# Kernel tuning notes

Hardware: AMD Instinct MI355X
Metric: run time of the kernel (lower is better)

## Reference

```python
import jax, jax.numpy as jnp
import numpy as np
import itertools

N_OBJECTS = 6  # subsets of range(6), sizes 1..6 -> 63 subsets

def _subset_groups():
    # group subsets by length so each group runs as one batched LSTM
    groups = {}
    for m in range(1, N_OBJECTS + 1):
        for s in itertools.combinations(range(6), m):
            groups.setdefault(m, []).append(list(s))
    return [(m, np.asarray(v, dtype=np.int32)) for m, v in groups.items()]

SUBSET_GROUPS = _subset_groups()


def _lstm_final_h(x, W_ih, W_hh, b_ih, b_hh):
    """x: [B,T,D] -> final hidden state [B,H]. PyTorch gate order i,f,g,o."""
    H = W_hh.shape[1]
    B = x.shape[0]
    # precompute input projections for all timesteps: [B,T,4H]
    xz = jnp.einsum('btd,gd->btg', x, W_ih) + b_ih + b_hh

    def step(carry, xt):
        h, c = carry
        z = xt + h @ W_hh.T
        i, f, g, o = jnp.split(z, 4, axis=-1)
        c = jax.nn.sigmoid(f) * c + jax.nn.sigmoid(i) * jnp.tanh(g)
        h = jax.nn.sigmoid(o) * jnp.tanh(c)
        return (h, c), None

    h0 = jnp.zeros((B, H), x.dtype)
    (h, _), _ = jax.lax.scan(step, (h0, h0), jnp.swapaxes(xz, 0, 1))
    return h


def setup_inputs() -> dict:
    key = jax.random.key(0)
    ks = jax.random.split(key, 10)
    D, H, FC, A = 16, 128, 256, 10
    mb = 8192
    s = lambda k, shape, fan: jax.random.normal(k, shape, jnp.float32) * (1.0 / np.sqrt(fan))
    return {
        'x_input': jax.random.normal(ks[0], (mb, 6, D), jnp.float32),
        'W_ih': s(ks[1], (4 * H, D), D),
        'W_hh': s(ks[2], (4 * H, H), H),
        'b_ih': jnp.zeros((4 * H,), jnp.float32),
        'b_hh': jnp.zeros((4 * H,), jnp.float32),
        'fc1_W': s(ks[3], (FC, H), H),
        'fc1_b': jnp.zeros((FC,), jnp.float32),
        'fc2_W': s(ks[4], (A, FC), FC),
        'fc2_b': jnp.zeros((A,), jnp.float32),
    }


def reference(x_input, W_ih, W_hh, b_ih, b_hh, fc1_W, fc1_b, fc2_W, fc2_b):
    mb = x_input.shape[0]
    H = W_hh.shape[1]
    hs = []
    # subsets of the same length are batched into one LSTM pass (fused form of
    # the original 63-iteration python loop); aggregation is permutation-invariant
    for m, idx in SUBSET_GROUPS:
        nL = idx.shape[0]
        xg = x_input[:, idx, :]                       # [mb, nL, m, D] gather
        xg = xg.reshape(mb * nL, m, x_input.shape[-1])
        h = _lstm_final_h(xg, W_ih, W_hh, b_ih, b_hh)  # [mb*nL, H]
        hs.append(h.reshape(mb, nL, H))
    holder = jnp.concatenate(hs, axis=1)              # [mb, 63, H]
    x = jnp.max(holder, axis=1)                       # aggregate == 'max'
    x = jax.nn.relu(x @ fc1_W.T + fc1_b)
    x = x @ fc2_W.T + fc2_b
    return jax.nn.log_softmax(x, axis=-1)
```

## Files before the change

kernel.cpp:

```cpp
#include <hip/hip_runtime.h>
#include <hip/hip_bf16.h>

#define BLOCK   512
#define NSAMP   16
#define HDIM    128
#define DDIM    16
#define NOBJ    6
#define NSLOT   16

typedef __attribute__((ext_vector_type(8))) short bf16x8;
typedef __attribute__((ext_vector_type(4))) float f32x4;

constexpr int pc6(int m)  { int c = 0; for (int i = 0; i < 6; ++i) c += (m >> i) & 1; return c; }
constexpr int msb6(int m) { int b = -1; for (int i = 0; i < 6; ++i) if (m & (1 << i)) b = i; return b; }

struct NodeRec { int jo, ps, sl; };
struct Plan { int cnt[7]; int n1[7]; NodeRec nd[7][20]; };
constexpr Plan make_plan() {
    Plan P{};
    int slotOf[64] = {};
    bool busy[NSLOT] = {};
    for (int d = 1; d <= 6; ++d) {
        int n = 0;
        for (int M = 1; M < 64; ++M) {
            if (pc6(M) != d || msb6(M) != 5) continue;
            P.nd[d][n].jo = 5;
            P.nd[d][n].ps = (d == 1) ? -1 : slotOf[M & ~(1 << 5)];
            P.nd[d][n].sl = -1;
            ++n;
        }
        int pend[20] = {}; int np = 0;
        for (int M = 1; M < 64; ++M) {
            if (pc6(M) != d || msb6(M) >= 5) continue;
            const int hi = msb6(M);
            int fs = -1;
            for (int s = 0; s < NSLOT; ++s) if (!busy[s]) { fs = s; break; }
            if (fs >= 0) {
                busy[fs] = true; slotOf[M] = fs;
                P.nd[d][n].jo = hi;
                P.nd[d][n].ps = (d == 1) ? -1 : slotOf[M & ~(1 << hi)];
                P.nd[d][n].sl = fs;
                ++n;
            } else pend[np++] = M;
        }
        P.n1[d] = n;
        int freeds[20] = {}; int nf = 0;
        if (d >= 2)
            for (int M = 1; M < 64; ++M)
                if (pc6(M) == d - 1 && msb6(M) == 4) freeds[nf++] = slotOf[M];
        for (int i = 0; i < np; ++i) {
            const int M = pend[i]; const int hi = msb6(M);
            const int s = freeds[--nf];
            slotOf[M] = s;
            P.nd[d][n].jo = hi;
            P.nd[d][n].ps = slotOf[M & ~(1 << hi)];
            P.nd[d][n].sl = s;
            ++n;
        }
        P.cnt[d] = n;
        for (int s = 0; s < NSLOT; ++s) busy[s] = false;
        for (int M = 1; M < 64; ++M)
            if (pc6(M) == d && msb6(M) < 5) busy[slotOf[M]] = true;
    }
    return P;
}
constexpr Plan PL = make_plan();

#define LOG2E   1.44269504f
#define TWOL2E  2.88539008f
#define SLOT_SH (16 * NSAMP * 8)

__device__ __forceinline__ unsigned short f2bf(float x) {
    union { float f; unsigned int u; } a; a.f = x;
    unsigned int r = (a.u + 0x7FFFu + ((a.u >> 16) & 1u)) >> 16;
    return (unsigned short)r;
}
__device__ __forceinline__ unsigned pk2(float a, float b) {
    union { __hip_bfloat162 h; unsigned u; } z;
    z.h = __float22bfloat162_rn(float2{a, b});
    return z.u;
}
__device__ __forceinline__ float bflo(unsigned p) {
    union { unsigned u; float f; } a; a.u = p << 16; return a.f;
}
__device__ __forceinline__ float bfhi(unsigned p) {
    union { unsigned u; float f; } a; a.u = p & 0xFFFF0000u; return a.f;
}


__global__ __launch_bounds__(BLOCK)
__attribute__((amdgpu_waves_per_eu(2, 4)))
void subset_lstm_fused_kernel(
    const float* __restrict__ x_input,
    const float* __restrict__ W_ih,
    const float* __restrict__ W_hh,
    const float* __restrict__ b_ih,
    const float* __restrict__ b_hh,
    const float* __restrict__ fc1_W,
    const float* __restrict__ fc1_b,
    const float* __restrict__ fc2_W,
    const float* __restrict__ fc2_b,
    float* __restrict__ out)
{
    __shared__ __align__(16) unsigned short hs[NSLOT * SLOT_SH];
    __shared__ __align__(16) unsigned short xb[NOBJ * 2 * NSAMP * 8];
    __shared__ __align__(16) unsigned short xpad[16];
    float* s_maxh  = (float*)hs;
    float* s_fc1   = (float*)(hs + 4096);
    float* s_logit = (float*)xb;

    const int t      = threadIdx.x;
    const int w      = t >> 6;
    const int lane   = t & 63;
    const int quad   = lane >> 4;
    const int m16    = lane & 15;
    const int s_base = blockIdx.x * NSAMP;

    if (t < 16) xpad[t] = (t == 0) ? f2bf(1.0f) : (unsigned short)0;

    for (int idx = t; idx < NOBJ * 2 * NSAMP * 8; idx += BLOCK) {
        const int j = idx & 7, n = (idx >> 3) & 15, q = (idx >> 7) & 1, obj = idx >> 8;
        xb[idx] = f2bf(x_input[(s_base + n) * (NOBJ * DDIM) + obj * DDIM + q * 8 + j]);
    }

    bf16x8 wf[4][5];
    #pragma unroll
    for (int g = 0; g < 4; ++g) {
        const float sc = (g == 2) ? TWOL2E : -LOG2E;
        const int grow = g * HDIM + w * 16 + m16;
        const float* whr = W_hh + grow * HDIM;
        const float* wir = W_ih + grow * DDIM;
        #pragma unroll
        for (int q = 0; q < 4; ++q) {
            union { unsigned short u[8]; bf16x8 v; } pk;
            #pragma unroll
            for (int j = 0; j < 8; ++j)
                pk.u[j] = f2bf(sc * whr[q * 32 + quad * 8 + j]);
            wf[g][q] = pk.v;
        }
        {
            union { unsigned short u[8]; bf16x8 v; } pk;
            #pragma unroll
            for (int j = 0; j < 8; ++j) {
                float v = 0.0f;
                if (quad < 2) v = sc * wir[quad * 8 + j];
                else if (quad == 2 && j == 0) v = sc * (b_ih[grow] + b_hh[grow]);
                pk.u[j] = f2bf(v);
            }
            wf[g][4] = pk.v;
        }
    }

    uint2 cs[NSLOT];
    float mh[4] = {-1e30f, -1e30f, -1e30f, -1e30f};
    const int kslot = w * 2 + (quad >> 1);

    #pragma unroll
    for (int d = 1; d <= 6; ++d) {
        __syncthreads();
        #pragma unroll
        for (int seg = 0; seg < 2; ++seg) {
            const int sBeg = seg ? PL.n1[d] : 0;
            const int sEnd = seg ? PL.cnt[d] : PL.n1[d];
            if (seg && sBeg >= sEnd) continue;
            if (seg) __syncthreads();

            #pragma unroll
            for (int ni = sBeg; ni < sEnd; ni += 2) {
                f32x4 acc[2][4];
                #pragma unroll
                for (int e = 0; e < 2; ++e) {
                    if (ni + e >= sEnd) continue;
                    const int jo = PL.nd[d][ni + e].jo;
                    const int ps = PL.nd[d][ni + e].ps;
                    #pragma unroll
                    for (int g = 0; g < 4; ++g)
                        acc[e][g] = f32x4{0.f, 0.f, 0.f, 0.f};
                    const unsigned short* bp = (quad < 2)
                        ? &xb[((jo * 2 + quad) * NSAMP + m16) * 8]
                        : &xpad[(quad - 2) * 8];
                    const bf16x8 bfx = *(const bf16x8*)bp;
                    #pragma unroll
                    for (int g = 0; g < 4; ++g)
                        acc[e][g] = __builtin_amdgcn_mfma_f32_16x16x32_bf16(
                            wf[g][4], bfx, acc[e][g], 0, 0, 0);
                    if (ps >= 0) {
                        #pragma unroll
                        for (int q = 0; q < 4; ++q) {
                            const bf16x8 bh = *(const bf16x8*)
                                &hs[((ps * 16 + q * 4 + quad) * NSAMP + m16) * 8];
                            #pragma unroll
                            for (int g = 0; g < 4; ++g)
                                acc[e][g] = __builtin_amdgcn_mfma_f32_16x16x32_bf16(
                                    wf[g][q], bh, acc[e][g], 0, 0, 0);
                        }
                    }
                }
                #pragma unroll
                for (int e = 0; e < 2; ++e) {
                    if (ni + e >= sEnd) continue;
                    const int ps = PL.nd[d][ni + e].ps;
                    const int sl = PL.nd[d][ni + e].sl;
                    float cn4[4], hn4[4];
                    #pragma unroll
                    for (int r = 0; r < 4; ++r) {
                        float cprev = 0.0f;
                        if (ps >= 0) {
                            const unsigned p = (r < 2) ? cs[ps].x : cs[ps].y;
                            cprev = (r & 1) ? bfhi(p) : bflo(p);
                        }
                        const float u  = 1.0f + __builtin_amdgcn_exp2f(acc[e][0][r]);
                        const float q  = 1.0f + __builtin_amdgcn_exp2f(acc[e][1][r]);
                        const float v  = 1.0f + __builtin_amdgcn_exp2f(acc[e][2][r]);
                        const float qo = 1.0f + __builtin_amdgcn_exp2f(acc[e][3][r]);
                        const float uv  = u * v;
                        const float num = fmaf(q, v - 2.0f, cprev * uv);
                        const float cn  = num * __builtin_amdgcn_rcpf(q * uv);
                        const float wt  = 1.0f + __builtin_amdgcn_exp2f(TWOL2E * cn);
                        const float h   = (wt - 2.0f) * __builtin_amdgcn_rcpf(qo * wt);
                        cn4[r] = cn; hn4[r] = h;
                        mh[r] = fmaxf(mh[r], h);
                    }
                    if (sl >= 0) {
                        cs[sl].x = pk2(cn4[0], cn4[1]);
                        cs[sl].y = pk2(cn4[2], cn4[3]);
                        union { __hip_bfloat162 h2[2]; uint2 v; } hp;
                        hp.h2[0] = __float22bfloat162_rn(float2{hn4[0], hn4[1]});
                        hp.h2[1] = __float22bfloat162_rn(float2{hn4[2], hn4[3]});
                        *(uint2*)&hs[((sl * 16 + kslot) * NSAMP + m16) * 8
                                     + (quad & 1) * 4] = hp.v;
                    }
                }
            }
        }
    }

    __syncthreads();
    {
        float4 v; v.x = mh[0]; v.y = mh[1]; v.z = mh[2]; v.w = mh[3];
        *(float4*)&s_maxh[m16 * HDIM + w * 16 + quad * 4] = v;
    }
    __syncthreads();

    {
        const int f  = t & 255;
        const int sh = t >> 8;
        float a1[8];
        #pragma unroll
        for (int s = 0; s < 8; ++s) a1[s] = fc1_b[f];
        for (int k4 = 0; k4 < HDIM / 4; ++k4) {
            const float4 wv = *(const float4*)&fc1_W[f * HDIM + k4 * 4];
            #pragma unroll
            for (int s = 0; s < 8; ++s) {
                const float4 h4 = *(const float4*)&s_maxh[(sh * 8 + s) * HDIM + k4 * 4];
                a1[s] += wv.x * h4.x + wv.y * h4.y + wv.z * h4.z + wv.w * h4.w;
            }
        }
        #pragma unroll
        for (int s = 0; s < 8; ++s)
            s_fc1[(sh * 8 + s) * 256 + f] = fmaxf(a1[s], 0.0f);
    }
    __syncthreads();

    if (t < NSAMP * 10) {
        const int s = t / 10, a = t % 10;
        float acc2 = fc2_b[a];
        for (int f4 = 0; f4 < 256 / 4; ++f4) {
            const float4 wv = *(const float4*)&fc2_W[a * 256 + f4 * 4];
            const float4 v  = *(const float4*)&s_fc1[s * 256 + f4 * 4];
            acc2 += wv.x * v.x + wv.y * v.y + wv.z * v.z + wv.w * v.w;
        }
        s_logit[s * 10 + a] = acc2;
    }
    __syncthreads();

    if (t < NSAMP) {
        float m = -1e30f;
        #pragma unroll
        for (int a = 0; a < 10; ++a) m = fmaxf(m, s_logit[t * 10 + a]);
        float sum = 0.0f;
        #pragma unroll
        for (int a = 0; a < 10; ++a) sum += __expf(s_logit[t * 10 + a] - m);
        const float lse = m + __logf(sum);
        #pragma unroll
        for (int a = 0; a < 10; ++a)
            out[(s_base + t) * 10 + a] = s_logit[t * 10 + a] - lse;
    }
}

extern "C" void kernel_launch(void* const* d_in, const int* in_sizes, int n_in,
                              void* d_out, int out_size, void* d_ws, size_t ws_size,
                              hipStream_t stream)
{
    (void)d_ws; (void)ws_size; (void)n_in; (void)out_size;

    const float* x   = (const float*)d_in[0];
    const float* Wih = (const float*)d_in[1];
    const float* Whh = (const float*)d_in[2];
    const float* bih = (const float*)d_in[3];
    const float* bhh = (const float*)d_in[4];
    const float* f1w = (const float*)d_in[5];
    const float* f1b = (const float*)d_in[6];
    const float* f2w = (const float*)d_in[7];
    const float* f2b = (const float*)d_in[8];

    const int mb = in_sizes[0] / (NOBJ * DDIM);
    dim3 grid(mb / NSAMP), block(BLOCK);
    subset_lstm_fused_kernel<<<grid, block, 0, stream>>>(
        x, Wih, Whh, bih, bhh, f1w, f1b, f2w, f2b, (float*)d_out);
}
```

Measured before the change: 204.2 us.

## Roll subset-LSTM schedule into table-driven loop with cell state in LDS

Replaces the fully unrolled compile-time plan with a rolled loop that reads packed node records from a kernel-argument table. Cell state moves from a 16-entry register array into shared memory, and the constant bias-pad row is folded into the x buffer. Nodes are now processed one at a time instead of in pairs, and the waves_per_eu hint is dropped. The aim is to cut code size and register pressure, at the cost of less MFMA interleaving between nodes plus extra LDS traffic and loop overhead.

```diff
diff --git a/kernel.cpp b/kernel.cpp
--- a/kernel.cpp
+++ b/kernel.cpp
@@ -66,9 +66,11 @@
 }
 constexpr Plan PL = make_plan();
 
+struct KTab { unsigned rec[63]; int cnt[8]; int n1[8]; };
+
 #define LOG2E   1.44269504f
 #define TWOL2E  2.88539008f
-#define SLOT_SH (16 * NSAMP * 8)
+#define SLOT_SH 2048
 
 __device__ __forceinline__ unsigned short f2bf(float x) {
     union { float f; unsigned int u; } a; a.f = x;
@@ -89,8 +91,7 @@
 
 
 __global__ __launch_bounds__(BLOCK)
-__attribute__((amdgpu_waves_per_eu(2, 4)))
-void subset_lstm_fused_kernel(
+void subset_lstm_rolled_kernel(
     const float* __restrict__ x_input,
     const float* __restrict__ W_ih,
     const float* __restrict__ W_hh,
@@ -100,11 +101,12 @@
     const float* __restrict__ fc1_b,
     const float* __restrict__ fc2_W,
     const float* __restrict__ fc2_b,
-    float* __restrict__ out)
+    float* __restrict__ out,
+    KTab tab)
 {
-    __shared__ __align__(16) unsigned short hs[NSLOT * SLOT_SH];
-    __shared__ __align__(16) unsigned short xb[NOBJ * 2 * NSAMP * 8];
-    __shared__ __align__(16) unsigned short xpad[16];
+    __shared__ __align__(16) unsigned short hs [NSLOT * SLOT_SH];
+    __shared__ __align__(16) unsigned short csb[NSLOT * SLOT_SH];
+    __shared__ __align__(16) unsigned short xb[NOBJ * 4 * NSAMP * 8];
     float* s_maxh  = (float*)hs;
     float* s_fc1   = (float*)(hs + 4096);
     float* s_logit = (float*)xb;
@@ -116,11 +118,12 @@
     const int m16    = lane & 15;
     const int s_base = blockIdx.x * NSAMP;
 
-    if (t < 16) xpad[t] = (t == 0) ? f2bf(1.0f) : (unsigned short)0;
-
-    for (int idx = t; idx < NOBJ * 2 * NSAMP * 8; idx += BLOCK) {
-        const int j = idx & 7, n = (idx >> 3) & 15, q = (idx >> 7) & 1, obj = idx >> 8;
-        xb[idx] = f2bf(x_input[(s_base + n) * (NOBJ * DDIM) + obj * DDIM + q * 8 + j]);
+    for (int idx = t; idx < NOBJ * 4 * NSAMP * 8; idx += BLOCK) {
+        const int j = idx & 7, n = (idx >> 3) & 15, q = (idx >> 7) & 3, obj = idx >> 9;
+        float v;
+        if (q < 2) v = x_input[(s_base + n) * (NOBJ * DDIM) + obj * DDIM + q * 8 + j];
+        else       v = (q == 2 && j == 0) ? 1.0f : 0.0f;
+        xb[idx] = f2bf(v);
     }
 
     bf16x8 wf[4][5];
@@ -151,88 +154,78 @@
         }
     }
 
-    uint2 cs[NSLOT];
+    unsigned short* const h_rd_lane = &hs [(quad * NSAMP + m16) * 8];
+    unsigned short* const h_wr_lane = &hs [(((w * 2 + (quad >> 1)) * NSAMP) + m16) * 8 + (quad & 1) * 4];
+    unsigned short* const c_lane    = &csb[(((w * 4 + quad) * NSAMP) + m16) * 4];
+    const f32x4 fzero = {0.f, 0.f, 0.f, 0.f};
+
     float mh[4] = {-1e30f, -1e30f, -1e30f, -1e30f};
-    const int kslot = w * 2 + (quad >> 1);
-
-    #pragma unroll
+    int base = 0;
+
+    #pragma clang loop unroll(disable)
     for (int d = 1; d <= 6; ++d) {
         __syncthreads();
-        #pragma unroll
-        for (int seg = 0; seg < 2; ++seg) {
-            const int sBeg = seg ? PL.n1[d] : 0;
-            const int sEnd = seg ? PL.cnt[d] : PL.n1[d];
-            if (seg && sBeg >= sEnd) continue;
-            if (seg) __syncthreads();
-
-            #pragma unroll
-            for (int ni = sBeg; ni < sEnd; ni += 2) {
-                f32x4 acc[2][4];
+        const int cnt = tab.cnt[d];
+        const int n1  = tab.n1[d];
+        #pragma clang loop unroll(disable)
+        for (int ni = 0; ni < cnt; ++ni) {
+            if (ni == n1) __syncthreads();
+            const unsigned rec = tab.rec[base + ni];
+            const int jo = (int)(rec & 7u);
+            const int ps = (int)((rec >> 3) & 31u) - 1;
+            const int sl = (int)((rec >> 8) & 31u) - 1;
+
+            float cp[4] = {0.f, 0.f, 0.f, 0.f};
+            if (ps >= 0) {
+                const uint2 cpk = *(const uint2*)(c_lane + ps * SLOT_SH);
+                cp[0] = bflo(cpk.x); cp[1] = bfhi(cpk.x);
+                cp[2] = bflo(cpk.y); cp[3] = bfhi(cpk.y);
+            }
+
+            f32x4 acc[4];
+            {
+                const bf16x8 bfx = *(const bf16x8*)&xb[((jo * 4 + quad) * NSAMP + m16) * 8];
                 #pragma unroll
-                for (int e = 0; e < 2; ++e) {
-                    if (ni + e >= sEnd) continue;
-                    const int jo = PL.nd[d][ni + e].jo;
-                    const int ps = PL.nd[d][ni + e].ps;
+                for (int g = 0; g < 4; ++g)
+                    acc[g] = __builtin_amdgcn_mfma_f32_16x16x32_bf16(
+                        wf[g][4], bfx, fzero, 0, 0, 0);
+            }
+            if (ps >= 0) {
+                const unsigned short* hb = h_rd_lane + ps * SLOT_SH;
+                #pragma unroll
+                for (int q = 0; q < 4; ++q) {
+                    const bf16x8 bh = *(const bf16x8*)(hb + q * (SLOT_SH / 4));
                     #pragma unroll
                     for (int g = 0; g < 4; ++g)
-                        acc[e][g] = f32x4{0.f, 0.f, 0.f, 0.f};
-                    const unsigned short* bp = (quad < 2)
-                        ? &xb[((jo * 2 + quad) * NSAMP + m16) * 8]
-                        : &xpad[(quad - 2) * 8];
-                    const bf16x8 bfx = *(const bf16x8*)bp;
-                    #pragma unroll
-                    for (int g = 0; g < 4; ++g)
-                        acc[e][g] = __builtin_amdgcn_mfma_f32_16x16x32_bf16(
-                            wf[g][4], bfx, acc[e][g], 0, 0, 0);
-                    if (ps >= 0) {
-                        #pragma unroll
-                        for (int q = 0; q < 4; ++q) {
-                            const bf16x8 bh = *(const bf16x8*)
-                                &hs[((ps * 16 + q * 4 + quad) * NSAMP + m16) * 8];
-                            #pragma unroll
-                            for (int g = 0; g < 4; ++g)
-                                acc[e][g] = __builtin_amdgcn_mfma_f32_16x16x32_bf16(
-                                    wf[g][q], bh, acc[e][g], 0, 0, 0);
-                        }
-                    }
+                        acc[g] = __builtin_amdgcn_mfma_f32_16x16x32_bf16(
+                            wf[g][q], bh, acc[g], 0, 0, 0);
                 }
-                #pragma unroll
-                for (int e = 0; e < 2; ++e) {
-                    if (ni + e >= sEnd) continue;
-                    const int ps = PL.nd[d][ni + e].ps;
-                    const int sl = PL.nd[d][ni + e].sl;
-                    float cn4[4], hn4[4];
-                    #pragma unroll
-                    for (int r = 0; r < 4; ++r) {
-                        float cprev = 0.0f;
-                        if (ps >= 0) {
-                            const unsigned p = (r < 2) ? cs[ps].x : cs[ps].y;
-                            cprev = (r & 1) ? bfhi(p) : bflo(p);
-                        }
-                        const float u  = 1.0f + __builtin_amdgcn_exp2f(acc[e][0][r]);
-                        const float q  = 1.0f + __builtin_amdgcn_exp2f(acc[e][1][r]);
-                        const float v  = 1.0f + __builtin_amdgcn_exp2f(acc[e][2][r]);
-                        const float qo = 1.0f + __builtin_amdgcn_exp2f(acc[e][3][r]);
-                        const float uv  = u * v;
-                        const float num = fmaf(q, v - 2.0f, cprev * uv);
-                        const float cn  = num * __builtin_amdgcn_rcpf(q * uv);
-                        const float wt  = 1.0f + __builtin_amdgcn_exp2f(TWOL2E * cn);
-                        const float h   = (wt - 2.0f) * __builtin_amdgcn_rcpf(qo * wt);
-                        cn4[r] = cn; hn4[r] = h;
-                        mh[r] = fmaxf(mh[r], h);
-                    }
-                    if (sl >= 0) {
-                        cs[sl].x = pk2(cn4[0], cn4[1]);
-                        cs[sl].y = pk2(cn4[2], cn4[3]);
-                        union { __hip_bfloat162 h2[2]; uint2 v; } hp;
-                        hp.h2[0] = __float22bfloat162_rn(float2{hn4[0], hn4[1]});
-                        hp.h2[1] = __float22bfloat162_rn(float2{hn4[2], hn4[3]});
-                        *(uint2*)&hs[((sl * 16 + kslot) * NSAMP + m16) * 8
-                                     + (quad & 1) * 4] = hp.v;
-                    }
-                }
-            }
-        }
+            }
+
+            float cn4[4], hn4[4];
+            #pragma unroll
+            for (int r = 0; r < 4; ++r) {
+                const float u  = 1.0f + __builtin_amdgcn_exp2f(acc[0][r]);
+                const float q  = 1.0f + __builtin_amdgcn_exp2f(acc[1][r]);
+                const float v  = 1.0f + __builtin_amdgcn_exp2f(acc[2][r]);
+                const float qo = 1.0f + __builtin_amdgcn_exp2f(acc[3][r]);
+                const float uv  = u * v;
+                const float num = fmaf(q, v - 2.0f, cp[r] * uv);
+                const float cn  = num * __builtin_amdgcn_rcpf(q * uv);
+                const float wt  = 1.0f + __builtin_amdgcn_exp2f(TWOL2E * cn);
+                const float h   = (wt - 2.0f) * __builtin_amdgcn_rcpf(qo * wt);
+                cn4[r] = cn; hn4[r] = h;
+                mh[r] = fmaxf(mh[r], h);
+            }
+
+            if (sl >= 0) {
+                uint2 cw; cw.x = pk2(cn4[0], cn4[1]); cw.y = pk2(cn4[2], cn4[3]);
+                *(uint2*)(c_lane + sl * SLOT_SH) = cw;
+                uint2 hw; hw.x = pk2(hn4[0], hn4[1]); hw.y = pk2(hn4[2], hn4[3]);
+                *(uint2*)(h_wr_lane + sl * SLOT_SH) = hw;
+            }
+        }
+        base += cnt;
     }
 
     __syncthreads();
@@ -293,6 +286,17 @@
                               hipStream_t stream)
 {
     (void)d_ws; (void)ws_size; (void)n_in; (void)out_size;
+
+    KTab tab{};
+    int k = 0;
+    for (int d = 1; d <= 6; ++d) {
+        tab.cnt[d] = PL.cnt[d];
+        tab.n1[d]  = (PL.n1[d] == PL.cnt[d]) ? 0x7fffffff : PL.n1[d];
+        for (int i = 0; i < PL.cnt[d]; ++i)
+            tab.rec[k++] = (unsigned)PL.nd[d][i].jo
+                         | ((unsigned)(PL.nd[d][i].ps + 1) << 3)
+                         | ((unsigned)(PL.nd[d][i].sl + 1) << 8);
+    }
 
     const float* x   = (const float*)d_in[0];
     const float* Wih = (const float*)d_in[1];
@@ -306,6 +310,6 @@
 
     const int mb = in_sizes[0] / (NOBJ * DDIM);
     dim3 grid(mb / NSAMP), block(BLOCK);
-    subset_lstm_fused_kernel<<<grid, block, 0, stream>>>(
-        x, Wih, Whh, bih, bhh, f1w, f1b, f2w, f2b, (float*)d_out);
-}
+    subset_lstm_rolled_kernel<<<grid, block, 0, stream>>>(
+        x, Wih, Whh, bih, bhh, f1w, f1b, f2w, f2b, (float*)d_out, tab);
+}
```

Result: slower. 222.9 us (+9.1%).

## Shrink prefix-state slots to 14 with barrier-phased slot reuse plan

Applied to the files above, without the earlier changes.

Rewrites the compile-time subset-tree plan so that only 14 hidden/cell state slots are needed. Slots whose children have all been placed are freed and reused within a level, with a barrier inserted before each reuse phase. The reduced slot count shrinks the per-thread packed cell-state registers and the LDS hidden buffer, which may allow higher occupancy. The node loop is also flattened to process one node at a time instead of pairs, which removes the two-node interleaving of MFMA chains and may add barriers.

```diff
diff --git a/kernel.cpp b/kernel.cpp
--- a/kernel.cpp
+++ b/kernel.cpp
@@ -6,7 +6,7 @@
 #define HDIM    128
 #define DDIM    16
 #define NOBJ    6
-#define NSLOT   16
+#define NSLOT   14
 
 typedef __attribute__((ext_vector_type(8))) short bf16x8;
 typedef __attribute__((ext_vector_type(4))) float f32x4;
@@ -14,61 +14,86 @@
 constexpr int pc6(int m)  { int c = 0; for (int i = 0; i < 6; ++i) c += (m >> i) & 1; return c; }
 constexpr int msb6(int m) { int b = -1; for (int i = 0; i < 6; ++i) if (m & (1 << i)) b = i; return b; }
 
-struct NodeRec { int jo, ps, sl; };
-struct Plan { int cnt[7]; int n1[7]; NodeRec nd[7][20]; };
-constexpr Plan make_plan() {
-    Plan P{};
+struct PNode { int jo, ps, sl; bool bar; };
+struct Plan2 { PNode nd[63]; int lvlStart[8]; };
+constexpr Plan2 make_plan2() {
+    Plan2 P{};
     int slotOf[64] = {};
     bool busy[NSLOT] = {};
+    int k = 0;
     for (int d = 1; d <= 6; ++d) {
-        int n = 0;
+        P.lvlStart[d] = k;
         for (int M = 1; M < 64; ++M) {
             if (pc6(M) != d || msb6(M) != 5) continue;
-            P.nd[d][n].jo = 5;
-            P.nd[d][n].ps = (d == 1) ? -1 : slotOf[M & ~(1 << 5)];
-            P.nd[d][n].sl = -1;
-            ++n;
+            P.nd[k].jo = 5;
+            P.nd[k].ps = (d == 1) ? -1 : slotOf[M & ~(1 << 5)];
+            P.nd[k].sl = -1;
+            P.nd[k].bar = false;
+            ++k;
         }
         int pend[20] = {}; int np = 0;
-        for (int M = 1; M < 64; ++M) {
-            if (pc6(M) != d || msb6(M) >= 5) continue;
-            const int hi = msb6(M);
-            int fs = -1;
-            for (int s = 0; s < NSLOT; ++s) if (!busy[s]) { fs = s; break; }
-            if (fs >= 0) {
+        for (int M = 1; M < 64; ++M)
+            if (pc6(M) == d && msb6(M) < 5) pend[np++] = M;
+        int key[20] = {};
+        for (int i = 0; i < np; ++i) {
+            if (d == 1) { key[i] = 0; continue; }
+            const int par = pend[i] & ~(1 << msb6(pend[i]));
+            int c2 = 0;
+            for (int j2 = 0; j2 < np; ++j2)
+                if ((pend[j2] & ~(1 << msb6(pend[j2]))) == par) ++c2;
+            key[i] = c2;
+        }
+        for (int a = 0; a < np; ++a)
+            for (int b2 = a + 1; b2 < np; ++b2)
+                if (key[b2] < key[a]) {
+                    int tm = key[a]; key[a] = key[b2]; key[b2] = tm;
+                    tm = pend[a]; pend[a] = pend[b2]; pend[b2] = tm;
+                }
+        bool placed[20] = {};
+        int nplaced = 0;
+        bool firstPhase = true;
+        while (nplaced < np) {
+            bool needBar = !firstPhase;
+            bool any = false;
+            for (int i = 0; i < np; ++i) {
+                if (placed[i]) continue;
+                int fs = -1;
+                for (int s = 0; s < NSLOT; ++s) if (!busy[s]) { fs = s; break; }
+                if (fs < 0) break;
+                const int M = pend[i]; const int hi = msb6(M);
                 busy[fs] = true; slotOf[M] = fs;
-                P.nd[d][n].jo = hi;
-                P.nd[d][n].ps = (d == 1) ? -1 : slotOf[M & ~(1 << hi)];
-                P.nd[d][n].sl = fs;
-                ++n;
-            } else pend[np++] = M;
-        }
-        P.n1[d] = n;
-        int freeds[20] = {}; int nf = 0;
-        if (d >= 2)
-            for (int M = 1; M < 64; ++M)
-                if (pc6(M) == d - 1 && msb6(M) == 4) freeds[nf++] = slotOf[M];
-        for (int i = 0; i < np; ++i) {
-            const int M = pend[i]; const int hi = msb6(M);
-            const int s = freeds[--nf];
-            slotOf[M] = s;
-            P.nd[d][n].jo = hi;
-            P.nd[d][n].ps = slotOf[M & ~(1 << hi)];
-            P.nd[d][n].sl = s;
-            ++n;
-        }
-        P.cnt[d] = n;
+                P.nd[k].jo = hi;
+                P.nd[k].ps = (d == 1) ? -1 : slotOf[M & ~(1 << hi)];
+                P.nd[k].sl = fs;
+                P.nd[k].bar = needBar; needBar = false;
+                ++k; placed[i] = true; ++nplaced; any = true;
+            }
+            firstPhase = false;
+            if (nplaced < np) {
+                if (!any) break;
+                for (int M = 1; M < 64; ++M) {
+                    if (pc6(M) != d - 1 || msb6(M) >= 5) continue;
+                    bool allp = true;
+                    for (int i = 0; i < np; ++i)
+                        if (!placed[i] &&
+                            ((pend[i] & ~(1 << msb6(pend[i]))) == M)) allp = false;
+                    if (allp) busy[slotOf[M]] = false;
+                }
+            }
+        }
         for (int s = 0; s < NSLOT; ++s) busy[s] = false;
         for (int M = 1; M < 64; ++M)
             if (pc6(M) == d && msb6(M) < 5) busy[slotOf[M]] = true;
     }
+    P.lvlStart[7] = k;
     return P;
 }
-constexpr Plan PL = make_plan();
+constexpr Plan2 PL2 = make_plan2();
+static_assert(PL2.lvlStart[7] == 63, "plan must cover all 63 nodes");
 
 #define LOG2E   1.44269504f
 #define TWOL2E  2.88539008f
-#define SLOT_SH (16 * NSAMP * 8)
+#define SLOT_SH 2048
 
 __device__ __forceinline__ unsigned short f2bf(float x) {
     union { float f; unsigned int u; } a; a.f = x;
@@ -90,7 +115,7 @@
 
 __global__ __launch_bounds__(BLOCK)
 __attribute__((amdgpu_waves_per_eu(2, 4)))
-void subset_lstm_fused_kernel(
+void subset_lstm_l14_kernel(
     const float* __restrict__ x_input,
     const float* __restrict__ W_ih,
     const float* __restrict__ W_hh,
@@ -159,78 +184,68 @@
     for (int d = 1; d <= 6; ++d) {
         __syncthreads();
         #pragma unroll
-        for (int seg = 0; seg < 2; ++seg) {
-            const int sBeg = seg ? PL.n1[d] : 0;
-            const int sEnd = seg ? PL.cnt[d] : PL.n1[d];
-            if (seg && sBeg >= sEnd) continue;
-            if (seg) __syncthreads();
-
-            #pragma unroll
-            for (int ni = sBeg; ni < sEnd; ni += 2) {
-                f32x4 acc[2][4];
+        for (int k = PL2.lvlStart[d]; k < PL2.lvlStart[d + 1]; ++k) {
+            if (PL2.nd[k].bar) __syncthreads();
+            const int jo = PL2.nd[k].jo;
+            const int ps = PL2.nd[k].ps;
+            const int sl = PL2.nd[k].sl;
+
+            f32x4 acc[4];
+            #pragma unroll
+            for (int g = 0; g < 4; ++g)
+                acc[g] = f32x4{0.f, 0.f, 0.f, 0.f};
+
+            {
+                const unsigned short* bp = (quad < 2)
+                    ? &xb[((jo * 2 + quad) * NSAMP + m16) * 8]
+                    : &xpad[(quad - 2) * 8];
+                const bf16x8 bfx = *(const bf16x8*)bp;
                 #pragma unroll
-                for (int e = 0; e < 2; ++e) {
-                    if (ni + e >= sEnd) continue;
-                    const int jo = PL.nd[d][ni + e].jo;
-                    const int ps = PL.nd[d][ni + e].ps;
+                for (int g = 0; g < 4; ++g)
+                    acc[g] = __builtin_amdgcn_mfma_f32_16x16x32_bf16(
+                        wf[g][4], bfx, acc[g], 0, 0, 0);
+            }
+            if (ps >= 0) {
+                #pragma unroll
+                for (int q = 0; q < 4; ++q) {
+                    const bf16x8 bh = *(const bf16x8*)
+                        &hs[((ps * 16 + q * 4 + quad) * NSAMP + m16) * 8];
                     #pragma unroll
                     for (int g = 0; g < 4; ++g)
-                        acc[e][g] = f32x4{0.f, 0.f, 0.f, 0.f};
-                    const unsigned short* bp = (quad < 2)
-                        ? &xb[((jo * 2 + quad) * NSAMP + m16) * 8]
-                        : &xpad[(quad - 2) * 8];
-                    const bf16x8 bfx = *(const bf16x8*)bp;
-                    #pragma unroll
-                    for (int g = 0; g < 4; ++g)
-                        acc[e][g] = __builtin_amdgcn_mfma_f32_16x16x32_bf16(
-                            wf[g][4], bfx, acc[e][g], 0, 0, 0);
-                    if (ps >= 0) {
-                        #pragma unroll
-                        for (int q = 0; q < 4; ++q) {
-                            const bf16x8 bh = *(const bf16x8*)
-                                &hs[((ps * 16 + q * 4 + quad) * NSAMP + m16) * 8];
-                            #pragma unroll
-                            for (int g = 0; g < 4; ++g)
-                                acc[e][g] = __builtin_amdgcn_mfma_f32_16x16x32_bf16(
-                                    wf[g][q], bh, acc[e][g], 0, 0, 0);
-                        }
-                    }
+                        acc[g] = __builtin_amdgcn_mfma_f32_16x16x32_bf16(
+                            wf[g][q], bh, acc[g], 0, 0, 0);
                 }
-                #pragma unroll
-                for (int e = 0; e < 2; ++e) {
-                    if (ni + e >= sEnd) continue;
-                    const int ps = PL.nd[d][ni + e].ps;
-                    const int sl = PL.nd[d][ni + e].sl;
-                    float cn4[4], hn4[4];
-                    #pragma unroll
-                    for (int r = 0; r < 4; ++r) {
-                        float cprev = 0.0f;
-                        if (ps >= 0) {
-                            const unsigned p = (r < 2) ? cs[ps].x : cs[ps].y;
-                            cprev = (r & 1) ? bfhi(p) : bflo(p);
-                        }
-                        const float u  = 1.0f + __builtin_amdgcn_exp2f(acc[e][0][r]);
-                        const float q  = 1.0f + __builtin_amdgcn_exp2f(acc[e][1][r]);
-                        const float v  = 1.0f + __builtin_amdgcn_exp2f(acc[e][2][r]);
-                        const float qo = 1.0f + __builtin_amdgcn_exp2f(acc[e][3][r]);
-                        const float uv  = u * v;
-                        const float num = fmaf(q, v - 2.0f, cprev * uv);
-                        const float cn  = num * __builtin_amdgcn_rcpf(q * uv);
-                        const float wt  = 1.0f + __builtin_amdgcn_exp2f(TWOL2E * cn);
-                        const float h   = (wt - 2.0f) * __builtin_amdgcn_rcpf(qo * wt);
-                        cn4[r] = cn; hn4[r] = h;
-                        mh[r] = fmaxf(mh[r], h);
-                    }
-                    if (sl >= 0) {
-                        cs[sl].x = pk2(cn4[0], cn4[1]);
-                        cs[sl].y = pk2(cn4[2], cn4[3]);
-                        union { __hip_bfloat162 h2[2]; uint2 v; } hp;
-                        hp.h2[0] = __float22bfloat162_rn(float2{hn4[0], hn4[1]});
-                        hp.h2[1] = __float22bfloat162_rn(float2{hn4[2], hn4[3]});
-                        *(uint2*)&hs[((sl * 16 + kslot) * NSAMP + m16) * 8
-                                     + (quad & 1) * 4] = hp.v;
-                    }
+            }
+
+            float cn4[4], hn4[4];
+            #pragma unroll
+            for (int r = 0; r < 4; ++r) {
+                float cprev = 0.0f;
+                if (ps >= 0) {
+                    const unsigned p = (r < 2) ? cs[ps].x : cs[ps].y;
+                    cprev = (r & 1) ? bfhi(p) : bflo(p);
                 }
+                const float u  = 1.0f + __builtin_amdgcn_exp2f(acc[0][r]);
+                const float q  = 1.0f + __builtin_amdgcn_exp2f(acc[1][r]);
+                const float v  = 1.0f + __builtin_amdgcn_exp2f(acc[2][r]);
+                const float qo = 1.0f + __builtin_amdgcn_exp2f(acc[3][r]);
+                const float uv  = u * v;
+                const float num = fmaf(q, v - 2.0f, cprev * uv);
+                const float cn  = num * __builtin_amdgcn_rcpf(q * uv);
+                const float wt  = 1.0f + __builtin_amdgcn_exp2f(TWOL2E * cn);
+                const float h   = (wt - 2.0f) * __builtin_amdgcn_rcpf(qo * wt);
+                cn4[r] = cn; hn4[r] = h;
+                mh[r] = fmaxf(mh[r], h);
+            }
+
+            if (sl >= 0) {
+                cs[sl].x = pk2(cn4[0], cn4[1]);
+                cs[sl].y = pk2(cn4[2], cn4[3]);
+                union { __hip_bfloat162 h2[2]; uint2 v; } hp;
+                hp.h2[0] = __float22bfloat162_rn(float2{hn4[0], hn4[1]});
+                hp.h2[1] = __float22bfloat162_rn(float2{hn4[2], hn4[3]});
+                *(uint2*)&hs[((sl * 16 + kslot) * NSAMP + m16) * 8
+                             + (quad & 1) * 4] = hp.v;
             }
         }
     }
@@ -306,6 +321,6 @@
 
     const int mb = in_sizes[0] / (NOBJ * DDIM);
     dim3 grid(mb / NSAMP), block(BLOCK);
-    subset_lstm_fused_kernel<<<grid, block, 0, stream>>>(
+    subset_lstm_l14_kernel<<<grid, block, 0, stream>>>(
         x, Wih, Whh, bih, bhh, f1w, f1b, f2w, f2b, (float*)d_out);
 }
```

New measurement: 196.9 us. 3.6% less time.
